# Kernel tuning notes

Measured on AMD Instinct MI355X. Metric: run time of the kernel, lower is better.

The kernel has to match this reference:

```python
import jax, jax.numpy as jnp
import numpy as np

B, N, C, H = 2, 2048, 768, 12
D = C // H
EPS = 1e-5


def setup_inputs() -> dict:
    key = jax.random.key(0)
    ks = jax.random.split(key, 12)
    s = 0.02
    return {
        "x": jax.random.normal(ks[0], (B, N, C), jnp.float32),
        "attn_mask": jax.random.randint(ks[1], (N, N), 0, 2) > 0,  # True = NOT allowed
        "ln1_g": jnp.ones((C,), jnp.float32),
        "ln1_b": jnp.zeros((C,), jnp.float32),
        "w_qkv": jax.random.normal(ks[2], (C, 3 * C), jnp.float32) * s,  # [in,out]
        "b_qkv": jnp.zeros((3 * C,), jnp.float32),
        "w_proj": jax.random.normal(ks[3], (C, C), jnp.float32) * s,
        "b_proj": jnp.zeros((C,), jnp.float32),
        "ls1": jnp.full((C,), 1e-5, jnp.float32),
        "ln2_g": jnp.ones((C,), jnp.float32),
        "ln2_b": jnp.zeros((C,), jnp.float32),
        "w1": jax.random.normal(ks[4], (C, 4 * C), jnp.float32) * s,
        "b1": jnp.zeros((4 * C,), jnp.float32),
        "w2": jax.random.normal(ks[5], (4 * C, C), jnp.float32) * s,
        "b2": jnp.zeros((C,), jnp.float32),
        "ls2": jnp.full((C,), 1e-5, jnp.float32),
    }


def layer_norm(x, g, b):
    mu = jnp.mean(x, axis=-1, keepdims=True)
    var = jnp.var(x, axis=-1, keepdims=True)
    return (x - mu) * jax.lax.rsqrt(var + EPS) * g + b


def reference(x, attn_mask, ln1_g, ln1_b, w_qkv, b_qkv, w_proj, b_proj, ls1,
              ln2_g, ln2_b, w1, b1, w2, b2, ls2):
    # ---- attention branch ----
    h = layer_norm(x, ln1_g, ln1_b)
    qkv = h @ w_qkv + b_qkv                       # [B,N,3C]
    qkv = qkv.reshape(B, N, 3, H, D).transpose(2, 0, 3, 1, 4)  # [3,B,H,N,D]
    q, k, v = qkv[0], qkv[1], qkv[2]
    scores = jnp.einsum('bhnd,bhmd->bhnm', q, k) * (D ** -0.5)  # [B,H,N,N]
    neg = jnp.finfo(scores.dtype).min
    scores = jnp.where(attn_mask, neg, scores)    # mask broadcasts over B,H
    attn = jax.nn.softmax(scores, axis=-1)
    o = jnp.einsum('bhnm,bhmd->bhnd', attn, v).transpose(0, 2, 1, 3).reshape(B, N, C)
    x = x + (o @ w_proj + b_proj) * ls1
    # ---- MLP branch ----
    h = layer_norm(x, ln2_g, ln2_b)
    h = jax.nn.gelu(h @ w1 + b1, approximate=False)
    x = x + (h @ w2 + b2) * ls2
    return x
```

## Files before the change

kernel.cpp:

```cpp
#include <hip/hip_runtime.h>
#include <hip/hip_bf16.h>
#include <math.h>

#define BN 2
#define SEQ 2048
#define CH 768
#define NH 12
#define HD 64
#define TOK (BN*SEQ)


using bf16_t = __hip_bfloat16;
typedef __attribute__((ext_vector_type(8))) short short8;
typedef __attribute__((ext_vector_type(8))) unsigned short ushort8;
typedef __attribute__((ext_vector_type(4))) float floatx4;
typedef __attribute__((ext_vector_type(2))) unsigned uintx2;

#define OFF_LN1G 0
#define OFF_LN1B 768
#define OFF_BQKV 1536
#define OFF_BPROJ 3840
#define OFF_LS1 4608
#define OFF_LN2G 5376
#define OFF_LN2B 6144
#define OFF_B1 6912
#define OFF_B2 9984
#define OFF_LS2 10752

__device__ inline float b2f(bf16_t v){ return __bfloat162float(v); }
__device__ inline bf16_t f2b(float v){ return __float2bfloat16(v); }
__device__ inline short f2bs(float v){ bf16_t b = __float2bfloat16(v); return *reinterpret_cast<short*>(&b); }
__device__ inline unsigned pk2(float a, float b){
  return (unsigned)(unsigned short)f2bs(a) | ((unsigned)(unsigned short)f2bs(b) << 16);
}
__device__ inline float sane(float v){ return (fabsf(v) < 1e30f) ? v : 0.0f; }
__device__ inline float clampf(float v, float lim){
  v = sane(v);
  return fminf(fmaxf(v, -lim), lim);
}
__device__ inline float ldf(const bf16_t* p){ return __bfloat162float(*p); }
__device__ inline float ldf(const float* p){ return *p; }
__device__ inline bool bf16_mode(const void* gref){
  return *reinterpret_cast<const unsigned*>(gref) == 0x3F803F80u;
}
__device__ inline void gload16(const void* g, void* l){
  __builtin_amdgcn_global_load_lds(
      (const __attribute__((address_space(1))) unsigned int*)g,
      (__attribute__((address_space(3))) unsigned int*)l, 16, 0, 0);
}

template<typename T>
__device__ inline void tr32(const T* __restrict__ src, size_t colOff, int stride,
    bf16_t* __restrict__ dst, int dstStride, int r0, int c0, float* smem, int tid)
{
  const int tx = tid & 31, ty = tid >> 5;
  #pragma unroll
  for (int j = 0; j < 4; j++)
    smem[(ty + j*8)*33 + tx] = ldf(src + (size_t)(r0 + ty + j*8) * stride + colOff + c0 + tx);
  __syncthreads();
  #pragma unroll
  for (int j = 0; j < 4; j++)
    dst[(size_t)(c0 + ty + j*8) * dstStride + r0 + tx] = f2b(smem[tx*33 + ty + j*8]);
}

template<typename T, bool GUARDED>
__global__ __launch_bounds__(256) void prep1_kernel(
    const T* __restrict__ x, const T* __restrict__ w_qkv, const T* __restrict__ w_proj,
    const T* __restrict__ w1, const T* __restrict__ w2,
    const T* __restrict__ g1, const T* __restrict__ b1_, const T* __restrict__ bqkv,
    const T* __restrict__ bproj, const T* __restrict__ ls1, const T* __restrict__ g2,
    const T* __restrict__ b2_, const T* __restrict__ bb1, const T* __restrict__ bb2,
    const T* __restrict__ ls2, const void* __restrict__ mask,
    float* __restrict__ pb, bf16_t* __restrict__ wqkvT, bf16_t* __restrict__ wprojT,
    unsigned long long* __restrict__ m1, bf16_t* __restrict__ a1,
    bf16_t* __restrict__ w1T, bf16_t* __restrict__ w2T,
    const void* __restrict__ gref)
{
  if (GUARDED && (bf16_mode(gref) != (sizeof(T) == 2))) return;
  __shared__ float smem[1056];
  const int tid = threadIdx.x;
  int wg = blockIdx.x;

  if (wg < 4096) {
    const T* xr = x + (size_t)wg * CH;
    float v0 = sane(ldf(xr + tid)), v1 = sane(ldf(xr + tid + 256)), v2 = sane(ldf(xr + tid + 512));
    float s  = v0 + v1 + v2;
    float s2 = v0*v0 + v1*v1 + v2*v2;
    #pragma unroll
    for (int o = 32; o > 0; o >>= 1) { s += __shfl_down(s, o, 64); s2 += __shfl_down(s2, o, 64); }
    if ((tid & 63) == 0) { smem[tid >> 6] = s; smem[(tid >> 6) + 4] = s2; }
    __syncthreads();
    if (tid == 0) {
      float ts = smem[0] + smem[1] + smem[2] + smem[3];
      float tq = smem[4] + smem[5] + smem[6] + smem[7];
      float mu = ts * (1.f / CH);
      float var = tq * (1.f / CH) - mu * mu;
      smem[8] = mu; smem[9] = rsqrtf(fmaxf(var, 0.f) + 1e-5f);
    }
    __syncthreads();
    const float mu = smem[8], rs = smem[9];
    bf16_t* orow = a1 + (size_t)wg * CH;
    orow[tid      ] = f2b(clampf((v0 - mu) * rs * ldf(g1 + tid      ) + ldf(b1_ + tid      ), 32.f));
    orow[tid + 256] = f2b(clampf((v1 - mu) * rs * ldf(g1 + tid + 256) + ldf(b1_ + tid + 256), 32.f));
    orow[tid + 512] = f2b(clampf((v2 - mu) * rs * ldf(g1 + tid + 512) + ldf(b1_ + tid + 512), 32.f));
    return;
  }
  wg -= 4096;
  if (wg < 1728) {
    tr32(w_qkv, 0, 2304, wqkvT, 768, (wg / 72) * 32, (wg % 72) * 32, smem, tid);
    return;
  }
  wg -= 1728;
  if (wg < 576) {
    tr32(w_proj, 0, 768, wprojT, 768, (wg / 24) * 32, (wg % 24) * 32, smem, tid);
    return;
  }
  wg -= 576;
  if (wg < 512) {
    const unsigned* mw = (const unsigned*)mask;
    unsigned accu = 0;
    #pragma unroll 8
    for (int i = 0; i < 64; i++) accu |= mw[i];
    const bool is8 = (accu > 1u);
    const int wave = tid >> 6, lane = tid & 63;
    #pragma unroll 4
    for (int i = 0; i < 32; i++) {
      const int word = wg * 128 + wave * 32 + i;
      const size_t elem = (size_t)word * 64 + lane;
      bool pred;
      if (is8) pred = ((const unsigned char*)mask)[elem] != 0;
      else     pred = ((const int*)mask)[elem] != 0;
      unsigned long long bits = __ballot(pred);
      if (lane == 0) m1[word] = bits;
    }
    return;
  }
  wg -= 512;
  if (wg < 1) {
    #define PCOPY(off, src, n) for (int i = tid; i < (n); i += 256) pb[(off)+i] = ldf((src)+i);
    PCOPY(OFF_LN1G, g1, 768)
    PCOPY(OFF_LN1B, b1_, 768)
    PCOPY(OFF_BQKV, bqkv, 2304)
    PCOPY(OFF_BPROJ, bproj, 768)
    PCOPY(OFF_LS1, ls1, 768)
    PCOPY(OFF_LN2G, g2, 768)
    PCOPY(OFF_LN2B, b2_, 768)
    PCOPY(OFF_B1, bb1, 3072)
    PCOPY(OFF_B2, bb2, 768)
    PCOPY(OFF_LS2, ls2, 768)
    #undef PCOPY
    return;
  }
  wg -= 1;
  if (wg < 2304) {
    tr32(w1, 0, 3072, w1T, 768, (wg / 96) * 32, (wg % 96) * 32, smem, tid);
    return;
  }
  wg -= 2304;
  {
    tr32(w2, 0, 768, w2T, 3072, (wg / 24) * 32, (wg % 24) * 32, smem, tid);
    return;
  }
}

template<typename T, bool GUARDED>
__global__ __launch_bounds__(256) void trc_kernel(const T* __restrict__ w1,
    const T* __restrict__ w2, bf16_t* __restrict__ w1Tc, bf16_t* __restrict__ w2Tc,
    int kc, const void* __restrict__ gref)
{
  if (GUARDED && (bf16_mode(gref) != (sizeof(T) == 2))) return;
  __shared__ float smem[1056];
  const int tid = threadIdx.x;
  int wg = blockIdx.x;
  if (wg < 576) {
    tr32(w1, (size_t)kc * 768, 3072, w1Tc, 768, (wg / 24) * 32, (wg % 24) * 32, smem, tid);
  } else {
    wg -= 576;
    tr32(w2 + (size_t)kc * 768 * 768, 0, 768, w2Tc, 768, (wg / 24) * 32, (wg % 24) * 32, smem, tid);
  }
}

__global__ __launch_bounds__(256) void ln2x_kernel(const bf16_t* __restrict__ x1,
    bf16_t* __restrict__ a2, const float* __restrict__ pb)
{
  __shared__ float red[10];
  const int row = blockIdx.x, tid = threadIdx.x;
  const bf16_t* xr = x1 + (size_t)row * CH;
  float v0 = sane(ldf(xr + tid)), v1 = sane(ldf(xr + tid + 256)), v2 = sane(ldf(xr + tid + 512));
  float s  = v0 + v1 + v2;
  float s2 = v0*v0 + v1*v1 + v2*v2;
  #pragma unroll
  for (int o = 32; o > 0; o >>= 1) { s += __shfl_down(s, o, 64); s2 += __shfl_down(s2, o, 64); }
  if ((tid & 63) == 0) { red[tid >> 6] = s; red[(tid >> 6) + 4] = s2; }
  __syncthreads();
  if (tid == 0) {
    float ts = red[0] + red[1] + red[2] + red[3];
    float tq = red[4] + red[5] + red[6] + red[7];
    float mu = ts * (1.f / CH);
    float var = tq * (1.f / CH) - mu * mu;
    red[8] = mu; red[9] = rsqrtf(fmaxf(var, 0.f) + 1e-5f);
  }
  __syncthreads();
  const float mu = red[8], rs = red[9];
  bf16_t* orow = a2 + (size_t)row * CH;
  orow[tid      ] = f2b(clampf((v0 - mu) * rs * pb[OFF_LN2G + tid      ] + pb[OFF_LN2B + tid      ], 32.f));
  orow[tid + 256] = f2b(clampf((v1 - mu) * rs * pb[OFF_LN2G + tid + 256] + pb[OFF_LN2B + tid + 256], 32.f));
  orow[tid + 512] = f2b(clampf((v2 - mu) * rs * pb[OFF_LN2G + tid + 512] + pb[OFF_LN2B + tid + 512], 32.f));
}

template<int MODE, int MT, int NT>
__global__ __launch_bounds__(256) void mgemm(
    const bf16_t* __restrict__ A, const bf16_t* __restrict__ BT,
    const float* __restrict__ pb, const int K, const int ldb,
    const int biasOff, const int scaleOff,
    const void* __restrict__ resid, const void* __restrict__ gref,
    bf16_t* __restrict__ o0, bf16_t* __restrict__ o1, bf16_t* __restrict__ vtout,
    float* __restrict__ oF, const bf16_t* __restrict__ stg,
    const int addPrev, const int finalize)
{
  constexpr int MI = MT / 32;
  constexpr int NI = NT / 32;
  constexpr int LOADS = MT / 64 + NT / 64;
  __shared__ __align__(16) short As[2][MT * 32];
  __shared__ __align__(16) short Bs[2][NT * 32];
  const int tid = threadIdx.x;
  const int wave = tid >> 6, lane = tid & 63, lane15 = lane & 15, quad = lane >> 4;
  const int wr = (wave >> 1) * (MT / 2), wc = (wave & 1) * (NT / 2);
  const int mBase = blockIdx.y * MT;
  const int nBase = blockIdx.x * NT;

  floatx4 acc[MI][NI];
  #pragma unroll
  for (int mi = 0; mi < MI; mi++)
    #pragma unroll
    for (int ni = 0; ni < NI; ni++) acc[mi][ni] = (floatx4){0.f, 0.f, 0.f, 0.f};

  const bf16_t* aS0 = A  + (size_t)(mBase + (tid >> 2)) * K + (tid & 3) * 8;
  const bf16_t* aS1 = aS0 + (size_t)64 * K;
  const bf16_t* bS0 = BT + (size_t)(nBase + (tid >> 2)) * ldb + (tid & 3) * 8;
  const bf16_t* bS1 = bS0 + (size_t)64 * ldb;
  const int wfl = __builtin_amdgcn_readfirstlane(wave);
  short* aD0 = &As[0][wfl * 512];
  short* aD1 = (MT == 128) ? &As[0][2048 + wfl * 512] : nullptr;
  short* bD0 = &Bs[0][wfl * 512];
  short* bD1 = (NT == 128) ? &Bs[0][2048 + wfl * 512] : nullptr;

  auto STAGE = [&](int buf, int k0) {
    const int ab = buf * (MT * 32), bb = buf * (NT * 32);
    gload16(aS0 + k0, aD0 + ab);
    if (MT == 128) gload16(aS1 + k0, aD1 + ab);
    gload16(bS0 + k0, bD0 + bb);
    if (NT == 128) gload16(bS1 + k0, bD1 + bb);
  };

  const int nsteps = K / 32;
  STAGE(0, 0);
  for (int t = 0; t < nsteps; ++t) {
    const int cur = t & 1;
    if (t + 1 < nsteps) {
      STAGE(cur ^ 1, (t + 1) * 32);
      if constexpr (LOADS == 2)      asm volatile("s_waitcnt vmcnt(2)" ::: "memory");
      else if constexpr (LOADS == 3) asm volatile("s_waitcnt vmcnt(3)" ::: "memory");
      else                           asm volatile("s_waitcnt vmcnt(4)" ::: "memory");
    } else {
      asm volatile("s_waitcnt vmcnt(0)" ::: "memory");
    }
    __builtin_amdgcn_s_barrier();
    short8 av[MI], bv[NI];
    #pragma unroll
    for (int mi = 0; mi < MI; mi++)
      av[mi] = *(const short8*)&As[cur][(wr + mi * 16 + lane15) * 32 + quad * 8];
    #pragma unroll
    for (int ni = 0; ni < NI; ni++)
      bv[ni] = *(const short8*)&Bs[cur][(wc + ni * 16 + lane15) * 32 + quad * 8];
    #pragma unroll
    for (int mi = 0; mi < MI; mi++)
      #pragma unroll
      for (int ni = 0; ni < NI; ni++)
        acc[mi][ni] = __builtin_amdgcn_mfma_f32_16x16x32_bf16(av[mi], bv[ni], acc[mi][ni], 0, 0, 0);
    __builtin_amdgcn_s_barrier();
  }

  const bool rbf = (MODE == 1) ? bf16_mode(gref) : false;
  #pragma unroll
  for (int mi = 0; mi < MI; mi++) {
    #pragma unroll
    for (int ni = 0; ni < NI; ni++) {
      const int c0u = nBase + wc + ni * 16;
      const int col = c0u + lane15;
      float bia = 0.f, sc = 0.f;
      if (MODE == 0 || MODE == 1 || MODE == 2) bia = pb[biasOff + col];
      if (MODE == 1) sc = pb[scaleOff + col];
      if (MODE == 3 && finalize) { bia = pb[biasOff + col]; sc = pb[scaleOff + col]; }
      if (MODE == 0 && c0u >= 2 * CH) {
        const int cv = col - 2 * CH;
        const int bh = (mBase >> 11) * NH + (cv >> 6);
        const int d = cv & 63;
        const int tok0 = (mBase + wr + mi * 16 + quad * 4) & (SEQ - 1);
        float tv[4];
        #pragma unroll
        for (int r = 0; r < 4; r++) tv[r] = clampf(acc[mi][ni][r] + bia, 20.f);
        uintx2 pk = (uintx2){ pk2(tv[0], tv[1]), pk2(tv[2], tv[3]) };
        *(uintx2*)(vtout + ((size_t)(bh * 64 + d)) * SEQ + tok0) = pk;
        continue;
      }
      #pragma unroll
      for (int r = 0; r < 4; r++) {
        const int row = mBase + wr + mi * 16 + quad * 4 + r;
        float v = acc[mi][ni][r];
        if (MODE == 0) {
          const bf16_t qv = f2b(clampf(v + bia, 20.f));
          if (col < CH) o0[(size_t)row * CH + col] = qv;
          else          o1[(size_t)row * CH + (col - CH)] = qv;
        } else if (MODE == 1) {
          const size_t ix = (size_t)row * CH + col;
          const float rx = rbf ? b2f(((const bf16_t*)resid)[ix]) : ((const float*)resid)[ix];
          const bf16_t xv = f2b(rx + clampf(sc * (v + bia), 0.5f));
          o0[ix] = xv;
          o1[ix] = xv;
        } else if (MODE == 2) {
          const float h = v + bia;
          const float g = 0.5f * h * (1.f + erff(h * 0.70710678118f));
          o0[(size_t)row * CH + col] = f2b(clampf(g, 50.f));
        } else {
          const size_t ix = (size_t)row * CH + col;
          if (addPrev) v += oF[ix];
          if (!finalize) oF[ix] = v;
          else oF[ix] = b2f(stg[ix]) + clampf(sc * (v + bia), 0.5f);
        }
      }
    }
  }
}

__global__ __launch_bounds__(256) void attn5_kernel(bf16_t* __restrict__ q,
    const bf16_t* __restrict__ kbuf, const bf16_t* __restrict__ vtb,
    const unsigned long long* __restrict__ m1)
{
  __shared__ __align__(16) short Ks[64 * 72];
  __shared__ __align__(16) short Vs[64 * 72];
  __shared__ unsigned Plds[4][32 * 17];
  const int bh = blockIdx.y, b = bh / NH, h = bh % NH;
  const int q0 = blockIdx.x * 64;
  const int tid = threadIdx.x;
  const int wave = tid >> 6, l15 = tid & 15, quad = (tid & 63) >> 4;
  const int srow = tid >> 2, scc = (tid & 3) * 16;
  const size_t kgbase = (size_t)(b * SEQ) * CH + h * HD;
  const size_t vgbase = (size_t)(bh * HD) * SEQ;
  const int qrow = q0 + wave * 16 + l15;

  short8 qf[2];
  {
    const unsigned short* qp = (const unsigned short*)q
        + (size_t)(b * SEQ + qrow) * CH + h * HD + quad * 8;
    qf[0] = *(const short8*)(qp);
    qf[1] = *(const short8*)(qp + 32);
  }
  const unsigned long long* mrow = m1 + (size_t)qrow * (SEQ / 64);

  float mreg = -1.1e4f, lreg = 0.f;
  floatx4 oacc[4] = {{0,0,0,0},{0,0,0,0},{0,0,0,0},{0,0,0,0}};
  unsigned* pw = &Plds[wave][0];

  const unsigned short* kp0 = (const unsigned short*)kbuf + kgbase + (size_t)srow * CH + scc;
  const unsigned short* vp0 = (const unsigned short*)vtb + vgbase + (size_t)srow * SEQ + scc;
  ushort8 kr0 = *(const ushort8*)(kp0);
  ushort8 kr1 = *(const ushort8*)(kp0 + 8);
  ushort8 vr0 = *(const ushort8*)(vp0);
  ushort8 vr1 = *(const ushort8*)(vp0 + 8);

  for (int k0 = 0; k0 < SEQ; k0 += 64) {
    __syncthreads();
    *(ushort8*)&Ks[srow * 72 + scc]     = kr0;
    *(ushort8*)&Ks[srow * 72 + scc + 8] = kr1;
    *(ushort8*)&Vs[srow * 72 + scc]     = vr0;
    *(ushort8*)&Vs[srow * 72 + scc + 8] = vr1;
    if (k0 + 64 < SEQ) {
      const unsigned short* kp = kp0 + (size_t)(k0 + 64) * CH;
      const unsigned short* vp = vp0 + (k0 + 64);
      kr0 = *(const ushort8*)(kp);
      kr1 = *(const ushort8*)(kp + 8);
      vr0 = *(const ushort8*)(vp);
      vr1 = *(const ushort8*)(vp + 8);
    }
    __syncthreads();

    const unsigned long long mw = mrow[k0 >> 6];
    float sv[4][4];
    float tmax = -1.0e30f;
    #pragma unroll
    for (int kb = 0; kb < 4; kb++) {
      floatx4 t = {0,0,0,0};
      short8 kf0 = *(const short8*)&Ks[(kb * 16 + l15) * 72 + quad * 8];
      short8 kf1 = *(const short8*)&Ks[(kb * 16 + l15) * 72 + 32 + quad * 8];
      __builtin_amdgcn_s_setprio(1);
      t = __builtin_amdgcn_mfma_f32_16x16x32_bf16(kf0, qf[0], t, 0, 0, 0);
      t = __builtin_amdgcn_mfma_f32_16x16x32_bf16(kf1, qf[1], t, 0, 0, 0);
      __builtin_amdgcn_s_setprio(0);
      #pragma unroll
      for (int r = 0; r < 4; r++) {
        float v = t[r] * 0.125f;
        if ((mw >> (kb * 16 + quad * 4 + r)) & 1ull) v = -1.0e30f;
        sv[kb][r] = v;
        tmax = fmaxf(tmax, v);
      }
    }
    tmax = fmaxf(tmax, __shfl_xor(tmax, 16, 64));
    tmax = fmaxf(tmax, __shfl_xor(tmax, 32, 64));

    if (__any(tmax > mreg)) {
      const float mnew = fmaxf(mreg, tmax);
      float alpha = __expf(mreg - mnew);
      alpha = (alpha <= 1.f) ? alpha : 0.f;
      lreg *= alpha;
      #pragma unroll
      for (int db = 0; db < 4; db++)
        #pragma unroll
        for (int r = 0; r < 4; r++) oacc[db][r] *= alpha;
      mreg = mnew;
    }

    float ls = 0.f;
    #pragma unroll
    for (int kb = 0; kb < 4; kb++) {
      float pr[4];
      #pragma unroll
      for (int r = 0; r < 4; r++) {
        const float pv = __expf(sv[kb][r] - mreg);
        pr[r] = pv;
        ls += pv;
      }
      pw[(8 * kb + 2 * quad)     * 17 + l15] = pk2(pr[0], pr[1]);
      pw[(8 * kb + 2 * quad + 1) * 17 + l15] = pk2(pr[2], pr[3]);
    }
    ls += __shfl_xor(ls, 16, 64);
    ls += __shfl_xor(ls, 32, 64);
    lreg += ls;

    #pragma unroll
    for (int s = 0; s < 2; s++) {
      union { unsigned u[4]; short8 s8; } pu;
      #pragma unroll
      for (int w = 0; w < 4; w++)
        pu.u[w] = pw[(16 * s + 4 * quad + w) * 17 + l15];
      __builtin_amdgcn_s_setprio(1);
      #pragma unroll
      for (int db = 0; db < 4; db++) {
        short8 vf = *(const short8*)&Vs[(db * 16 + l15) * 72 + s * 32 + quad * 8];
        oacc[db] = __builtin_amdgcn_mfma_f32_16x16x32_bf16(vf, pu.s8, oacc[db], 0, 0, 0);
      }
      __builtin_amdgcn_s_setprio(0);
    }
  }

  const float inv = 1.f / fmaxf(lreg, 1e-20f);
  unsigned short* op = (unsigned short*)q
      + (size_t)(b * SEQ + qrow) * CH + h * HD + quad * 4;
  #pragma unroll
  for (int db = 0; db < 4; db++) {
    const unsigned lo = pk2(clampf(oacc[db][0] * inv, 10.f), clampf(oacc[db][1] * inv, 10.f));
    const unsigned hi = pk2(clampf(oacc[db][2] * inv, 10.f), clampf(oacc[db][3] * inv, 10.f));
    *(uintx2*)(op + db * 16) = (uintx2){lo, hi};
  }
}

extern "C" void kernel_launch(void* const* d_in, const int* in_sizes, int n_in,
                              void* d_out, int out_size, void* d_ws, size_t ws_size,
                              hipStream_t stream) {
  const void* x      = d_in[0];
  const void* mask   = d_in[1];
  const void* ln1_g  = d_in[2];
  const void* ln1_b  = d_in[3];
  const void* w_qkv  = d_in[4];
  const void* b_qkv  = d_in[5];
  const void* w_proj = d_in[6];
  const void* b_proj = d_in[7];
  const void* ls1    = d_in[8];
  const void* ln2_g  = d_in[9];
  const void* ln2_b  = d_in[10];
  const void* w1     = d_in[11];
  const void* b1     = d_in[12];
  const void* w2     = d_in[13];
  const void* b2     = d_in[14];
  const void* ls2    = d_in[15];
  const void* gref   = ln1_g;

  char* ws = (char*)d_ws;
  float*  pb     = (float*)ws;
  bf16_t* a12    = (bf16_t*)(ws + 65536);
  bf16_t* vt     = (bf16_t*)(ws + 65536 + 6291456);
  bf16_t* stage  = vt;
  char*   r3     = ws + 65536 + 2 * 6291456;
  bf16_t* wqkvT  = (bf16_t*)r3;
  bf16_t* wprojT = (bf16_t*)(r3 + 3538944);
  bf16_t* hact   = (bf16_t*)r3;
  char*   r4     = ws + 65536 + 3 * 6291456;
  unsigned long long* mi1 = (unsigned long long*)r4;
  bf16_t* w1Tc   = (bf16_t*)r4;
  bf16_t* w2Tc   = (bf16_t*)(r4 + 1179648);
  char*   r5     = ws + 21299200;
  bf16_t* w1T    = (bf16_t*)r5;
  bf16_t* w2T    = (bf16_t*)(r5 + 4718592);
  bf16_t* dQ     = (bf16_t*)d_out;
  bf16_t* dK     = dQ + 3145728;
  float*  outF   = (float*)d_out;

  const long long xs = in_sizes ? (long long)in_sizes[0] : 0;
  const int mode = (xs == 6291456LL) ? 1 : (xs == 12582912LL ? 2 : 0);
  const bool doFull = (ws_size >= 30736384ULL);
  const int prepGrid = doFull ? 11521 : 6913;

  #define PREP_ARGS(T) (const T*)x, (const T*)w_qkv, (const T*)w_proj, (const T*)w1, (const T*)w2, \
      (const T*)ln1_g, (const T*)ln1_b, (const T*)b_qkv, (const T*)b_proj, (const T*)ls1, \
      (const T*)ln2_g, (const T*)ln2_b, (const T*)b1, (const T*)b2, (const T*)ls2, \
      mask, pb, wqkvT, wprojT, mi1, a12, w1T, w2T, gref
  if (mode == 1)      prep1_kernel<bf16_t, false><<<prepGrid, 256, 0, stream>>>(PREP_ARGS(bf16_t));
  else if (mode == 2) prep1_kernel<float,  false><<<prepGrid, 256, 0, stream>>>(PREP_ARGS(float));
  else {
    prep1_kernel<bf16_t, true><<<prepGrid, 256, 0, stream>>>(PREP_ARGS(bf16_t));
    prep1_kernel<float,  true><<<prepGrid, 256, 0, stream>>>(PREP_ARGS(float));
  }
  #undef PREP_ARGS

  mgemm<0, 128, 128><<<dim3(18, 32), 256, 0, stream>>>(a12, wqkvT, pb, 768, 768, OFF_BQKV, 0,
      nullptr, gref, dQ, dK, vt, nullptr, nullptr, 0, 0);
  attn5_kernel<<<dim3(SEQ / 64, BN * NH), 256, 0, stream>>>(dQ, dK, vt, mi1);
  mgemm<1, 64, 64><<<dim3(12, 64), 256, 0, stream>>>(dQ, wprojT, pb, 768, 768, OFF_BPROJ, OFF_LS1,
      x, gref, dK, stage, nullptr, nullptr, nullptr, 0, 0);
  ln2x_kernel<<<TOK, 256, 0, stream>>>(dK, a12, pb);
  for (int kc = 0; kc < 4; kc++) {
    const bf16_t* bt1; const bf16_t* bt2; int ldb2;
    if (doFull) {
      bt1 = w1T + (size_t)kc * 768 * 768;
      bt2 = w2T + (size_t)kc * 768;
      ldb2 = 3072;
    } else {
      if (mode == 1)      trc_kernel<bf16_t, false><<<1152, 256, 0, stream>>>((const bf16_t*)w1, (const bf16_t*)w2, w1Tc, w2Tc, kc, gref);
      else if (mode == 2) trc_kernel<float,  false><<<1152, 256, 0, stream>>>((const float*)w1,  (const float*)w2,  w1Tc, w2Tc, kc, gref);
      else {
        trc_kernel<bf16_t, true><<<1152, 256, 0, stream>>>((const bf16_t*)w1, (const bf16_t*)w2, w1Tc, w2Tc, kc, gref);
        trc_kernel<float,  true><<<1152, 256, 0, stream>>>((const float*)w1,  (const float*)w2,  w1Tc, w2Tc, kc, gref);
      }
      bt1 = w1Tc; bt2 = w2Tc; ldb2 = 768;
    }
    mgemm<2, 64, 64><<<dim3(12, 64), 256, 0, stream>>>(a12, bt1, pb, 768, 768, OFF_B1 + kc * 768, 0,
        nullptr, gref, hact, nullptr, nullptr, nullptr, nullptr, 0, 0);
    mgemm<3, 64, 64><<<dim3(12, 64), 256, 0, stream>>>(hact, bt2, pb, 768, ldb2, OFF_B2, OFF_LS2,
        nullptr, gref, nullptr, nullptr, nullptr, outF, stage, kc > 0 ? 1 : 0, kc == 3 ? 1 : 0);
  }
}
```

Before: 420.3 us.

## Double-buffer attention K/V tiles, restructure GEMM sync, fold softmax scale into Q

New measurement: 419.1 us. No clear change (-0.3%).

```diff
diff --git a/kernel.cpp b/kernel.cpp
--- a/kernel.cpp
+++ b/kernel.cpp
@@ -220,7 +220,6 @@
 {
   constexpr int MI = MT / 32;
   constexpr int NI = NT / 32;
-  constexpr int LOADS = MT / 64 + NT / 64;
   __shared__ __align__(16) short As[2][MT * 32];
   __shared__ __align__(16) short Bs[2][NT * 32];
   const int tid = threadIdx.x;
@@ -254,18 +253,12 @@
   };
 
   const int nsteps = K / 32;
+  int cur = 0;
   STAGE(0, 0);
+  asm volatile("s_waitcnt vmcnt(0)" ::: "memory");
+  __builtin_amdgcn_s_barrier();
   for (int t = 0; t < nsteps; ++t) {
-    const int cur = t & 1;
-    if (t + 1 < nsteps) {
-      STAGE(cur ^ 1, (t + 1) * 32);
-      if constexpr (LOADS == 2)      asm volatile("s_waitcnt vmcnt(2)" ::: "memory");
-      else if constexpr (LOADS == 3) asm volatile("s_waitcnt vmcnt(3)" ::: "memory");
-      else                           asm volatile("s_waitcnt vmcnt(4)" ::: "memory");
-    } else {
-      asm volatile("s_waitcnt vmcnt(0)" ::: "memory");
-    }
-    __builtin_amdgcn_s_barrier();
+    if (t + 1 < nsteps) STAGE(cur ^ 1, (t + 1) * 32);
     short8 av[MI], bv[NI];
     #pragma unroll
     for (int mi = 0; mi < MI; mi++)
@@ -278,7 +271,11 @@
       #pragma unroll
       for (int ni = 0; ni < NI; ni++)
         acc[mi][ni] = __builtin_amdgcn_mfma_f32_16x16x32_bf16(av[mi], bv[ni], acc[mi][ni], 0, 0, 0);
-    __builtin_amdgcn_s_barrier();
+    if (t + 1 < nsteps) {
+      asm volatile("s_waitcnt vmcnt(0)" ::: "memory");
+      __builtin_amdgcn_s_barrier();
+      cur ^= 1;
+    }
   }
 
   const bool rbf = (MODE == 1) ? bf16_mode(gref) : false;
@@ -309,9 +306,9 @@
         const int row = mBase + wr + mi * 16 + quad * 4 + r;
         float v = acc[mi][ni][r];
         if (MODE == 0) {
-          const bf16_t qv = f2b(clampf(v + bia, 20.f));
-          if (col < CH) o0[(size_t)row * CH + col] = qv;
-          else          o1[(size_t)row * CH + (col - CH)] = qv;
+          const float cv = clampf(v + bia, 20.f);
+          if (col < CH) o0[(size_t)row * CH + col] = f2b(cv * 0.125f);
+          else          o1[(size_t)row * CH + (col - CH)] = f2b(cv);
         } else if (MODE == 1) {
           const size_t ix = (size_t)row * CH + col;
           const float rx = rbf ? b2f(((const bf16_t*)resid)[ix]) : ((const float*)resid)[ix];
@@ -333,12 +330,12 @@
   }
 }
 
-__global__ __launch_bounds__(256) void attn5_kernel(bf16_t* __restrict__ q,
+__global__ __launch_bounds__(256) void attn6_kernel(bf16_t* __restrict__ q,
     const bf16_t* __restrict__ kbuf, const bf16_t* __restrict__ vtb,
     const unsigned long long* __restrict__ m1)
 {
-  __shared__ __align__(16) short Ks[64 * 72];
-  __shared__ __align__(16) short Vs[64 * 72];
+  __shared__ __align__(16) short Ks[2][64 * 72];
+  __shared__ __align__(16) short Vs[2][64 * 72];
   __shared__ unsigned Plds[4][32 * 17];
   const int bh = blockIdx.y, b = bh / NH, h = bh % NH;
   const int q0 = blockIdx.x * 64;
@@ -364,18 +361,24 @@
 
   const unsigned short* kp0 = (const unsigned short*)kbuf + kgbase + (size_t)srow * CH + scc;
   const unsigned short* vp0 = (const unsigned short*)vtb + vgbase + (size_t)srow * SEQ + scc;
-  ushort8 kr0 = *(const ushort8*)(kp0);
-  ushort8 kr1 = *(const ushort8*)(kp0 + 8);
-  ushort8 vr0 = *(const ushort8*)(vp0);
-  ushort8 vr1 = *(const ushort8*)(vp0 + 8);
-
+
+  {
+    ushort8 k0r = *(const ushort8*)(kp0);
+    ushort8 k1r = *(const ushort8*)(kp0 + 8);
+    ushort8 v0r = *(const ushort8*)(vp0);
+    ushort8 v1r = *(const ushort8*)(vp0 + 8);
+    *(ushort8*)&Ks[0][srow * 72 + scc]     = k0r;
+    *(ushort8*)&Ks[0][srow * 72 + scc + 8] = k1r;
+    *(ushort8*)&Vs[0][srow * 72 + scc]     = v0r;
+    *(ushort8*)&Vs[0][srow * 72 + scc + 8] = v1r;
+  }
+  __syncthreads();
+
+  int cur = 0;
+  ushort8 kr0, kr1, vr0, vr1;
   for (int k0 = 0; k0 < SEQ; k0 += 64) {
-    __syncthreads();
-    *(ushort8*)&Ks[srow * 72 + scc]     = kr0;
-    *(ushort8*)&Ks[srow * 72 + scc + 8] = kr1;
-    *(ushort8*)&Vs[srow * 72 + scc]     = vr0;
-    *(ushort8*)&Vs[srow * 72 + scc + 8] = vr1;
-    if (k0 + 64 < SEQ) {
+    const bool more = (k0 + 64 < SEQ);
+    if (more) {
       const unsigned short* kp = kp0 + (size_t)(k0 + 64) * CH;
       const unsigned short* vp = vp0 + (k0 + 64);
       kr0 = *(const ushort8*)(kp);
@@ -383,7 +386,6 @@
       vr0 = *(const ushort8*)(vp);
       vr1 = *(const ushort8*)(vp + 8);
     }
-    __syncthreads();
 
     const unsigned long long mw = mrow[k0 >> 6];
     float sv[4][4];
@@ -391,15 +393,15 @@
     #pragma unroll
     for (int kb = 0; kb < 4; kb++) {
       floatx4 t = {0,0,0,0};
-      short8 kf0 = *(const short8*)&Ks[(kb * 16 + l15) * 72 + quad * 8];
-      short8 kf1 = *(const short8*)&Ks[(kb * 16 + l15) * 72 + 32 + quad * 8];
+      short8 kf0 = *(const short8*)&Ks[cur][(kb * 16 + l15) * 72 + quad * 8];
+      short8 kf1 = *(const short8*)&Ks[cur][(kb * 16 + l15) * 72 + 32 + quad * 8];
       __builtin_amdgcn_s_setprio(1);
       t = __builtin_amdgcn_mfma_f32_16x16x32_bf16(kf0, qf[0], t, 0, 0, 0);
       t = __builtin_amdgcn_mfma_f32_16x16x32_bf16(kf1, qf[1], t, 0, 0, 0);
       __builtin_amdgcn_s_setprio(0);
       #pragma unroll
       for (int r = 0; r < 4; r++) {
-        float v = t[r] * 0.125f;
+        float v = t[r];
         if ((mw >> (kb * 16 + quad * 4 + r)) & 1ull) v = -1.0e30f;
         sv[kb][r] = v;
         tmax = fmaxf(tmax, v);
@@ -446,10 +448,19 @@
       __builtin_amdgcn_s_setprio(1);
       #pragma unroll
       for (int db = 0; db < 4; db++) {
-        short8 vf = *(const short8*)&Vs[(db * 16 + l15) * 72 + s * 32 + quad * 8];
+        short8 vf = *(const short8*)&Vs[cur][(db * 16 + l15) * 72 + s * 32 + quad * 8];
         oacc[db] = __builtin_amdgcn_mfma_f32_16x16x32_bf16(vf, pu.s8, oacc[db], 0, 0, 0);
       }
       __builtin_amdgcn_s_setprio(0);
+    }
+
+    if (more) {
+      *(ushort8*)&Ks[cur ^ 1][srow * 72 + scc]     = kr0;
+      *(ushort8*)&Ks[cur ^ 1][srow * 72 + scc + 8] = kr1;
+      *(ushort8*)&Vs[cur ^ 1][srow * 72 + scc]     = vr0;
+      *(ushort8*)&Vs[cur ^ 1][srow * 72 + scc + 8] = vr1;
+      __syncthreads();
+      cur ^= 1;
     }
   }
 
@@ -524,7 +535,7 @@
 
   mgemm<0, 128, 128><<<dim3(18, 32), 256, 0, stream>>>(a12, wqkvT, pb, 768, 768, OFF_BQKV, 0,
       nullptr, gref, dQ, dK, vt, nullptr, nullptr, 0, 0);
-  attn5_kernel<<<dim3(SEQ / 64, BN * NH), 256, 0, stream>>>(dQ, dK, vt, mi1);
+  attn6_kernel<<<dim3(SEQ / 64, BN * NH), 256, 0, stream>>>(dQ, dK, vt, mi1);
   mgemm<1, 64, 64><<<dim3(12, 64), 256, 0, stream>>>(dQ, wprojT, pb, 768, 768, OFF_BPROJ, OFF_LS1,
       x, gref, dK, stage, nullptr, nullptr, nullptr, 0, 0);
   ln2x_kernel<<<TOK, 256, 0, stream>>>(dK, a12, pb);
```
